# Optimization experiments

Hardware: AMD Instinct MI355X
Metric: run time of the kernel (lower is better)

Reference implementation:

```python
import jax, jax.numpy as jnp
import numpy as np

DIM = 32          # d_model == channel dim of the volume
D_STATE = 16
D_CONV = 4
EXPAND = 2
D_INNER = EXPAND * DIM        # 64
DT_RANK = max(1, (DIM + 15) // 16)  # ceil(d_model/16) = 2
LN_EPS = 1e-5


def setup_inputs() -> dict:
    key = jax.random.key(0)
    ks = jax.random.split(key, 12)
    B, Dd, Hh, Ww = 1, 32, 32, 32
    sc = 0.02
    x = jax.random.normal(ks[0], (B, DIM, Dd, Hh, Ww), jnp.float32)
    ln_w = jnp.ones((DIM,), jnp.float32)
    ln_b = jnp.zeros((DIM,), jnp.float32)
    in_proj_w = jax.random.normal(ks[1], (2 * D_INNER, DIM), jnp.float32) * sc
    conv_w = jax.random.normal(ks[2], (D_INNER, 1, D_CONV), jnp.float32) * sc
    conv_b = jnp.zeros((D_INNER,), jnp.float32)
    x_proj_w = jax.random.normal(ks[3], (DT_RANK + 2 * D_STATE, D_INNER), jnp.float32) * sc
    dt_proj_w = jax.random.normal(ks[4], (D_INNER, DT_RANK), jnp.float32) * sc
    dt_proj_b = jax.random.uniform(ks[5], (D_INNER,), jnp.float32, -4.0, -2.0)  # small softplus(dt) at init
    # Mamba S4D-real init: A = -[1..d_state], stored as A_log
    A_log = jnp.log(jnp.broadcast_to(jnp.arange(1, D_STATE + 1, dtype=jnp.float32), (D_INNER, D_STATE)))
    D_param = jnp.ones((D_INNER,), jnp.float32)
    out_proj_w = jax.random.normal(ks[6], (DIM, D_INNER), jnp.float32) * sc
    return {
        "x": x, "ln_w": ln_w, "ln_b": ln_b, "in_proj_w": in_proj_w,
        "conv_w": conv_w, "conv_b": conv_b, "x_proj_w": x_proj_w,
        "dt_proj_w": dt_proj_w, "dt_proj_b": dt_proj_b, "A_log": A_log,
        "D_param": D_param, "out_proj_w": out_proj_w,
    }


def _mamba_layer(x, ln_w, ln_b, in_proj_w, conv_w, conv_b, x_proj_w,
                 dt_proj_w, dt_proj_b, A_log, D_param, out_proj_w):
    B, C, Dd, Hh, Ww = x.shape
    L = Dd * Hh * Ww
    # z-scan flatten: (B, C, D, H, W) -> (B, L, C)
    xf = x.reshape(B, C, L).transpose(0, 2, 1)
    # LayerNorm over channel dim
    mu = jnp.mean(xf, axis=-1, keepdims=True)
    var = jnp.mean(jnp.square(xf - mu), axis=-1, keepdims=True)
    xn = (xf - mu) * jax.lax.rsqrt(var + LN_EPS) * ln_w + ln_b
    # in_proj -> x, z branches
    xz = xn @ in_proj_w.T                      # (B, L, 2*d_inner)
    x_in, z = jnp.split(xz, 2, axis=-1)
    # depthwise causal conv1d over sequence
    xt = x_in.transpose(0, 2, 1)               # (B, d_inner, L)
    xc = jax.lax.conv_general_dilated(
        xt, conv_w, window_strides=(1,), padding=[(D_CONV - 1, 0)],
        feature_group_count=D_INNER)
    xc = jax.nn.silu(xc + conv_b[None, :, None]).transpose(0, 2, 1)  # (B, L, d_inner)
    # input-dependent dt, B, C
    x_dbl = xc @ x_proj_w.T                    # (B, L, dt_rank + 2*d_state)
    dt, Bm, Cm = jnp.split(x_dbl, [DT_RANK, DT_RANK + D_STATE], axis=-1)
    delta = jax.nn.softplus(dt @ dt_proj_w.T + dt_proj_b)            # (B, L, d_inner)
    A = -jnp.exp(A_log)                        # (d_inner, d_state)
    # discretize: h_t = exp(delta*A) h_{t-1} + delta*B_t*x_t
    dA = jnp.exp(delta[..., None] * A)                               # (B, L, d_inner, d_state)
    dBx = delta[..., None] * Bm[:, :, None, :] * xc[..., None]       # (B, L, d_inner, d_state)
    def comb(e1, e2):
        a1, b1 = e1
        a2, b2 = e2
        return (a1 * a2, a2 * b1 + b2)
    _, h = jax.lax.associative_scan(comb, (dA, dBx), axis=1)         # parallel linear recurrence
    y = jnp.einsum('blds,bls->bld', h, Cm) + xc * D_param            # (B, L, d_inner)
    y = y * jax.nn.silu(z)
    out = y @ out_proj_w.T                     # (B, L, C)
    # unpermute z-scan
    return out.transpose(0, 2, 1).reshape(B, C, Dd, Hh, Ww)


def reference(x, ln_w, ln_b, in_proj_w, conv_w, conv_b, x_proj_w,
              dt_proj_w, dt_proj_b, A_log, D_param, out_proj_w):
    return _mamba_layer(x, ln_w, ln_b, in_proj_w, conv_w, conv_b, x_proj_w,
                        dt_proj_w, dt_proj_b, A_log, D_param, out_proj_w)
```

## Files before the change

### kernel.cpp

```cpp
#include <hip/hip_runtime.h>
#include <hip/hip_bf16.h>

constexpr int L   = 32768;
constexpr int CD  = 32;
constexpr int DI  = 64;
constexpr int DS  = 16;
constexpr int LC  = 64;
constexpr int NCH = L / LC;
constexpr int NPAIR = DI * DS;

constexpr size_t FL        = (size_t)DI * L;
constexpr size_t OFF_SZ    = 0;
constexpr size_t OFF_XC    = FL;
constexpr size_t OFF_DELTA = 2 * FL;
constexpr size_t OFF_BM    = 3 * FL;
constexpr size_t OFF_CM    = OFF_BM + (size_t)DS * L;
constexpr size_t OFF_APROD = OFF_CM + (size_t)DS * L;
constexpr size_t OFF_CARRY = OFF_APROD;
constexpr size_t OFF_BACC  = OFF_APROD + (size_t)NCH * NPAIR;

__device__ __forceinline__ float bf2f(__hip_bfloat16 v) { return __bfloat162float(v); }
__device__ __forceinline__ void f4arr(const float4 v, float* a) { a[0]=v.x; a[1]=v.y; a[2]=v.z; a[3]=v.w; }

__device__ __forceinline__ bool detect_bf16(const void* ln_w) {
    return ((const unsigned short*)ln_w)[0] == 0x3F80;
}
__device__ __forceinline__ float ldin(const void* p, size_t i, bool bf16) {
    return bf16 ? bf2f(((const __hip_bfloat16*)p)[i]) : ((const float*)p)[i];
}

__global__ __launch_bounds__(256) void k12_featurize_scan(
    const void* __restrict__ x,
    const void* __restrict__ ln_w,
    const void* __restrict__ ln_b,
    const void* __restrict__ in_proj_w,
    const void* __restrict__ conv_w,
    const void* __restrict__ conv_b,
    const void* __restrict__ x_proj_w,
    const void* __restrict__ dt_proj_w,
    const void* __restrict__ dt_proj_b,
    const void* __restrict__ A_log,
    float* __restrict__ ws)
{
    __shared__ __align__(16) char smem[67840];
    float (*xin_s)[69]  = (float(*)[69])(smem);
    char* AR = smem + 17664;
    float (*xn_s)[33]   = (float(*)[33])(AR);
    float (*w_in_s)[32] = (float(*)[32])(AR + 8848);
    float (*sdl)[68]    = (float(*)[68])(AR);
    float (*sxc)[68]    = (float(*)[68])(AR + 17408);
    float (*sbm)[68]    = (float(*)[68])(AR + 34816);
    char* FW = smem + 56832;
    float (*w_xp)[64]   = (float(*)[64])(FW);
    float (*w_cv)[4]    = (float(*)[4])(FW + 8704);
    float (*w_dt)[2]    = (float(*)[2])(FW + 9728);
    float* b_dt_s = (float*)(FW + 10240);
    float* b_cv_s = (float*)(FW + 10496);
    float* lnw_s  = (float*)(FW + 10752);
    float* lnb_s  = (float*)(FW + 10880);

    const int tid = threadIdx.x;
    const int l0  = blockIdx.x * LC;
    const bool isb = detect_bf16(ln_w);

    if (isb) {
        const __hip_bfloat16* ipw = (const __hip_bfloat16*)in_proj_w;
        const __hip_bfloat16* xpw = (const __hip_bfloat16*)x_proj_w;
        for (int i = tid; i < 128 * 32; i += 256) w_in_s[i >> 5][i & 31] = bf2f(ipw[i]);
        for (int i = tid; i < 34 * 64; i += 256)  w_xp[i >> 6][i & 63] = bf2f(xpw[i]);
    } else {
        const float* ipw = (const float*)in_proj_w;
        const float* xpw = (const float*)x_proj_w;
        for (int i = tid; i < 128 * 32; i += 256) w_in_s[i >> 5][i & 31] = ipw[i];
        for (int i = tid; i < 34 * 64; i += 256)  w_xp[i >> 6][i & 63] = xpw[i];
    }
    w_cv[tid >> 2][tid & 3] = ldin(conv_w, tid, isb);
    if (tid < 128) w_dt[tid >> 1][tid & 1] = ldin(dt_proj_w, tid, isb);
    if (tid < 64) { b_dt_s[tid] = ldin(dt_proj_b, tid, isb); b_cv_s[tid] = ldin(conv_b, tid, isb); }
    if (tid < 32) { lnw_s[tid] = ldin(ln_w, tid, isb); lnb_s[tid] = ldin(ln_b, tid, isb); }
    __syncthreads();

    if (tid < LC + 3) {
        const int l = l0 - 3 + tid;
        const bool valid = (l >= 0);
        const int lc = valid ? l : 0;
        float xv[CD];
        if (isb) {
            const __hip_bfloat16* xb = (const __hip_bfloat16*)x;
            #pragma unroll
            for (int c = 0; c < CD; ++c) xv[c] = bf2f(xb[(size_t)c * L + lc]);
        } else {
            const float* xf = (const float*)x;
            #pragma unroll
            for (int c = 0; c < CD; ++c) xv[c] = xf[(size_t)c * L + lc];
        }
        float mu = 0.f;
        #pragma unroll
        for (int c = 0; c < CD; ++c) mu += xv[c];
        mu *= (1.f / CD);
        float var = 0.f;
        #pragma unroll
        for (int c = 0; c < CD; ++c) { const float dc = xv[c] - mu; var += dc * dc; }
        const float rstd = rsqrtf(var * (1.f / CD) + 1e-5f);
        #pragma unroll
        for (int c = 0; c < CD; ++c)
            xn_s[tid][c] = valid ? ((xv[c] - mu) * rstd * lnw_s[c] + lnb_s[c]) : 0.f;
    }
    __syncthreads();

    {
        const int wv   = tid >> 6;
        const int lane = tid & 63;
        const int jb   = wv * 32;
        float xv[CD];
        if (wv < 2) {
            #pragma unroll
            for (int it = 0; it < 2; ++it) {
                const int pos = it * 64 + lane;
                if (pos < LC + 3) {
                    #pragma unroll
                    for (int c = 0; c < CD; ++c) xv[c] = xn_s[pos][c];
                    for (int j = 0; j < 32; ++j) {
                        const float4* wr = (const float4*)w_in_s[jb + j];
                        float acc = 0.f;
                        #pragma unroll
                        for (int q = 0; q < 8; ++q) {
                            const float4 w4 = wr[q];
                            acc += w4.x * xv[4*q] + w4.y * xv[4*q+1]
                                 + w4.z * xv[4*q+2] + w4.w * xv[4*q+3];
                        }
                        xin_s[jb + j][pos] = acc;
                    }
                }
            }
        } else {
            const int l = l0 + lane;
            #pragma unroll
            for (int c = 0; c < CD; ++c) xv[c] = xn_s[3 + lane][c];
            for (int j = 0; j < 32; ++j) {
                const float4* wr = (const float4*)w_in_s[jb + j];
                float acc = 0.f;
                #pragma unroll
                for (int q = 0; q < 8; ++q) {
                    const float4 w4 = wr[q];
                    acc += w4.x * xv[4*q] + w4.y * xv[4*q+1]
                         + w4.z * xv[4*q+2] + w4.w * xv[4*q+3];
                }
                const float s = acc / (1.f + __expf(-acc));
                ws[OFF_SZ + (size_t)(jb - 64 + j) * L + l] = s;
            }
        }
    }
    __syncthreads();

    {
        const int h  = tid & 3;
        const int pq = tid >> 2;
        const int l  = l0 + pq;
        const int dbase = h * 16;
        float xcv[16];
        #pragma unroll
        for (int i = 0; i < 16; ++i) {
            const int d = dbase + i;
            float acc = b_cv_s[d];
            #pragma unroll
            for (int k = 0; k < 4; ++k) acc += w_cv[d][k] * xin_s[d][pq + k];
            const float v = acc / (1.f + __expf(-acc));
            xcv[i] = v;
            ws[OFF_XC + (size_t)d * L + l] = v;
            sxc[d][pq] = v;
        }
        float dt0 = 0.f, dt1 = 0.f;
        for (int r = 0; r < 34; ++r) {
            float acc = 0.f;
            #pragma unroll
            for (int i = 0; i < 16; ++i) acc += w_xp[r][dbase + i] * xcv[i];
            acc += __shfl_xor(acc, 1);
            acc += __shfl_xor(acc, 2);
            if (r == 0) dt0 = acc;
            else if (r == 1) dt1 = acc;
            else {
                const int rr = r - 2;
                if (h == (rr >> 3)) {
                    const size_t off = (rr < 16) ? (OFF_BM + (size_t)rr * L)
                                                 : (OFF_CM + (size_t)(rr - 16) * L);
                    ws[off + l] = acc;
                    if (rr < 16) sbm[rr][pq] = acc;
                }
            }
        }
        #pragma unroll
        for (int i = 0; i < 16; ++i) {
            const int d = dbase + i;
            const float tv = dt0 * w_dt[d][0] + dt1 * w_dt[d][1] + b_dt_s[d];
            const float sp = fmaxf(tv, 0.f) + log1pf(__expf(-fabsf(tv)));
            ws[OFF_DELTA + (size_t)d * L + l] = sp;
            sdl[d][pq] = sp;
        }
    }
    __syncthreads();

    {
        const int d = tid >> 2, sg = tid & 3;
        float Aj[4], ap[4] = {1.f, 1.f, 1.f, 1.f}, bb[4] = {0.f, 0.f, 0.f, 0.f};
        #pragma unroll
        for (int j = 0; j < 4; ++j) Aj[j] = -__expf(ldin(A_log, d * DS + sg + 4 * j, isb));

        for (int t = 0; t < LC; t += 4) {
            float ddv[4], xxv[4], bm[4][4];
            f4arr(*(const float4*)&sdl[d][t], ddv);
            f4arr(*(const float4*)&sxc[d][t], xxv);
            f4arr(*(const float4*)&sbm[sg][t],      bm[0]);
            f4arr(*(const float4*)&sbm[sg + 4][t],  bm[1]);
            f4arr(*(const float4*)&sbm[sg + 8][t],  bm[2]);
            f4arr(*(const float4*)&sbm[sg + 12][t], bm[3]);
            #pragma unroll
            for (int tt = 0; tt < 4; ++tt) {
                const float dxc = ddv[tt] * xxv[tt];
                #pragma unroll
                for (int j = 0; j < 4; ++j) {
                    const float e = __expf(ddv[tt] * Aj[j]);
                    ap[j] *= e;
                    bb[j] = e * bb[j] + dxc * bm[j][tt];
                }
            }
        }
        const size_t o = (size_t)blockIdx.x * NPAIR + tid * 4;
        *(float4*)&ws[OFF_APROD + o] = make_float4(ap[0], ap[1], ap[2], ap[3]);
        *(float4*)&ws[OFF_BACC + o]  = make_float4(bb[0], bb[1], bb[2], bb[3]);
    }
}

__global__ __launch_bounds__(256) void k3_carry(float* __restrict__ ws)
{
    const int lane = threadIdx.x & 63;
    const int p    = (blockIdx.x * 256 + threadIdx.x) >> 6;

    float a[8], b[8];
    #pragma unroll
    for (int i = 0; i < 8; ++i) {
        const size_t c = (size_t)(lane * 8 + i);
        a[i] = ws[OFF_APROD + c * NPAIR + p];
        b[i] = ws[OFF_BACC  + c * NPAIR + p];
    }
    float Ag = a[0], Bg = b[0];
    #pragma unroll
    for (int i = 1; i < 8; ++i) { Bg = a[i] * Bg + b[i]; Ag = Ag * a[i]; }
    #pragma unroll
    for (int off = 1; off < 64; off <<= 1) {
        const float pa = __shfl_up(Ag, off);
        const float pb = __shfl_up(Bg, off);
        if (lane >= off) { Bg = Ag * pb + Bg; Ag = Ag * pa; }
    }
    float Pb = __shfl_up(Bg, 1);
    if (lane == 0) Pb = 0.f;
    #pragma unroll
    for (int i = 0; i < 8; ++i) {
        const size_t c = (size_t)(lane * 8 + i);
        ws[OFF_CARRY + c * NPAIR + p] = Pb;
        Pb = a[i] * Pb + b[i];
    }
}

__global__ __launch_bounds__(256) void k45_apply_out(
    const void* __restrict__ A_log,
    const void* __restrict__ D_param,
    const void* __restrict__ ln_w,
    const void* __restrict__ out_proj_w,
    float* __restrict__ ws,
    void* __restrict__ out)
{
    __shared__ __align__(16) float sdl[DI][68];
    __shared__ __align__(16) float sxc[DI][68];
    __shared__ __align__(16) float sbm[DS][68];
    __shared__ __align__(16) float scm[DS][68];
    __shared__ __align__(16) float sy[DI][68];
    __shared__ float w_out_s[CD][DI];
    const int tid = threadIdx.x;
    const int c   = blockIdx.x;
    const size_t t0 = (size_t)c * LC;
    const bool isb = detect_bf16(ln_w);

    if (isb) {
        const __hip_bfloat16* opw = (const __hip_bfloat16*)out_proj_w;
        for (int i = tid; i < CD * DI; i += 256) w_out_s[i >> 6][i & 63] = bf2f(opw[i]);
    } else {
        const float* opw = (const float*)out_proj_w;
        for (int i = tid; i < CD * DI; i += 256) w_out_s[i >> 6][i & 63] = opw[i];
    }
    for (int i = tid; i < DI * LC; i += 256) { const int r = i >> 6, t = i & 63; sdl[r][t] = ws[OFF_DELTA + (size_t)r * L + t0 + t]; }
    for (int i = tid; i < DI * LC; i += 256) { const int r = i >> 6, t = i & 63; sxc[r][t] = ws[OFF_XC + (size_t)r * L + t0 + t]; }
    for (int i = tid; i < DS * LC; i += 256) { const int r = i >> 6, t = i & 63; sbm[r][t] = ws[OFF_BM + (size_t)r * L + t0 + t]; }
    for (int i = tid; i < DS * LC; i += 256) { const int r = i >> 6, t = i & 63; scm[r][t] = ws[OFF_CM + (size_t)r * L + t0 + t]; }

    const int d = tid >> 2, sg = tid & 3;
    float Aj[4];
    #pragma unroll
    for (int j = 0; j < 4; ++j) Aj[j] = -__expf(ldin(A_log, d * DS + sg + 4 * j, isb));
    const float Dd = ldin(D_param, d, isb);
    const float4 h4 = *(const float4*)&ws[OFF_CARRY + (size_t)c * NPAIR + tid * 4];
    float hh[4]; f4arr(h4, hh);
    __syncthreads();

    for (int t = 0; t < LC; t += 4) {
        float ddv[4], xxv[4], bm[4][4], cm[4][4];
        f4arr(*(const float4*)&sdl[d][t], ddv);
        f4arr(*(const float4*)&sxc[d][t], xxv);
        f4arr(*(const float4*)&sbm[sg][t],      bm[0]);
        f4arr(*(const float4*)&sbm[sg + 4][t],  bm[1]);
        f4arr(*(const float4*)&sbm[sg + 8][t],  bm[2]);
        f4arr(*(const float4*)&sbm[sg + 12][t], bm[3]);
        f4arr(*(const float4*)&scm[sg][t],      cm[0]);
        f4arr(*(const float4*)&scm[sg + 4][t],  cm[1]);
        f4arr(*(const float4*)&scm[sg + 8][t],  cm[2]);
        f4arr(*(const float4*)&scm[sg + 12][t], cm[3]);
        #pragma unroll
        for (int tt = 0; tt < 4; ++tt) {
            const float dxc = ddv[tt] * xxv[tt];
            float ys = 0.f;
            #pragma unroll
            for (int j = 0; j < 4; ++j) {
                const float e = __expf(ddv[tt] * Aj[j]);
                hh[j] = e * hh[j] + dxc * bm[j][tt];
                ys += hh[j] * cm[j][tt];
            }
            ys += __shfl_xor(ys, 1);
            ys += __shfl_xor(ys, 2);
            if (sg == 0) sy[d][t + tt] = ys + xxv[tt] * Dd;
        }
    }
    __syncthreads();

    #pragma unroll
    for (int k = 0; k < 4; ++k) {
        const int idx = tid + k * 256;
        const int r = idx >> 4, t4 = (idx & 15) * 4;
        float4 yv = *(float4*)&sy[r][t4];
        const float4 zv = *(const float4*)&ws[OFF_SZ + (size_t)r * L + t0 + t4];
        yv.x *= zv.x; yv.y *= zv.y; yv.z *= zv.z; yv.w *= zv.w;
        *(float4*)&sy[r][t4] = yv;
    }
    __syncthreads();

    {
        const int wv   = tid >> 6;
        const int lane = tid & 63;
        float acc[8] = {0.f, 0.f, 0.f, 0.f, 0.f, 0.f, 0.f, 0.f};
        for (int dd = 0; dd < DI; ++dd) {
            const float yv = sy[dd][lane];
            #pragma unroll
            for (int j = 0; j < 8; ++j)
                acc[j] += yv * w_out_s[wv * 8 + j][dd];
        }
        const size_t l = t0 + lane;
        #pragma unroll
        for (int j = 0; j < 8; ++j) {
            const int cc = wv * 8 + j;
            if (isb) ((__hip_bfloat16*)out)[(size_t)cc * L + l] = __float2bfloat16(acc[j]);
            else     ((float*)out)[(size_t)cc * L + l] = acc[j];
        }
    }
}

extern "C" void kernel_launch(void* const* d_in, const int* in_sizes, int n_in,
                              void* d_out, int out_size, void* d_ws, size_t ws_size,
                              hipStream_t stream)
{
    (void)in_sizes; (void)n_in; (void)out_size; (void)ws_size;
    const void* x        = d_in[0];
    const void* ln_w     = d_in[1];
    const void* ln_b     = d_in[2];
    const void* in_pw    = d_in[3];
    const void* conv_w   = d_in[4];
    const void* conv_b   = d_in[5];
    const void* x_pw     = d_in[6];
    const void* dt_pw    = d_in[7];
    const void* dt_pb    = d_in[8];
    const void* A_log    = d_in[9];
    const void* D_param  = d_in[10];
    const void* out_pw   = d_in[11];
    float* ws = (float*)d_ws;

    k12_featurize_scan<<<NCH, 256, 0, stream>>>(x, ln_w, ln_b, in_pw, conv_w, conv_b,
                                                x_pw, dt_pw, dt_pb, A_log, ws);
    k3_carry<<<NPAIR / 4, 256, 0, stream>>>(ws);
    k45_apply_out<<<NCH, 256, 0, stream>>>(A_log, D_param, ln_w, out_pw, ws, d_out);
}
```

Baseline: 165.7 us.

## Transpose chunk-summary layout, vectorize carry scan, stream delta/xc from global

Chunk summaries (A products and B accumulators) and carries are now stored pair-major (p*NCH + chunk), so the carry kernel reads and writes contiguous float4 rows instead of strided scalars. The apply kernel drops its shared-memory staging of delta and xc and instead prefetches them from global one float4 ahead; it also gains a launch_bounds occupancy hint. In the in_proj stage, each thread now computes two positions per weight-row pass so the weights are read once. The trade-off is strided scalar stores in the chunk kernel and scattered carry loads in the apply kernel, plus global-load latency inside the scan loop.

```diff
diff --git a/kernel.cpp b/kernel.cpp
--- a/kernel.cpp
+++ b/kernel.cpp
@@ -112,29 +112,28 @@
         const int wv   = tid >> 6;
         const int lane = tid & 63;
         const int jb   = wv * 32;
-        float xv[CD];
         if (wv < 2) {
-            #pragma unroll
-            for (int it = 0; it < 2; ++it) {
-                const int pos = it * 64 + lane;
-                if (pos < LC + 3) {
-                    #pragma unroll
-                    for (int c = 0; c < CD; ++c) xv[c] = xn_s[pos][c];
-                    for (int j = 0; j < 32; ++j) {
-                        const float4* wr = (const float4*)w_in_s[jb + j];
-                        float acc = 0.f;
-                        #pragma unroll
-                        for (int q = 0; q < 8; ++q) {
-                            const float4 w4 = wr[q];
-                            acc += w4.x * xv[4*q] + w4.y * xv[4*q+1]
-                                 + w4.z * xv[4*q+2] + w4.w * xv[4*q+3];
-                        }
-                        xin_s[jb + j][pos] = acc;
-                    }
+            const int pos1  = 64 + lane;
+            const bool v1   = (pos1 < LC + 3);
+            const int pos1c = v1 ? pos1 : 66;
+            float xv0[CD], xv1[CD];
+            #pragma unroll
+            for (int c = 0; c < CD; ++c) { xv0[c] = xn_s[lane][c]; xv1[c] = xn_s[pos1c][c]; }
+            for (int j = 0; j < 32; ++j) {
+                const float4* wr = (const float4*)w_in_s[jb + j];
+                float a0 = 0.f, a1 = 0.f;
+                #pragma unroll
+                for (int q = 0; q < 8; ++q) {
+                    const float4 w4 = wr[q];
+                    a0 += w4.x * xv0[4*q] + w4.y * xv0[4*q+1] + w4.z * xv0[4*q+2] + w4.w * xv0[4*q+3];
+                    a1 += w4.x * xv1[4*q] + w4.y * xv1[4*q+1] + w4.z * xv1[4*q+2] + w4.w * xv1[4*q+3];
                 }
+                xin_s[jb + j][lane] = a0;
+                if (v1) xin_s[jb + j][pos1] = a1;
             }
         } else {
             const int l = l0 + lane;
+            float xv[CD];
             #pragma unroll
             for (int c = 0; c < CD; ++c) xv[c] = xn_s[3 + lane][c];
             for (int j = 0; j < 32; ++j) {
@@ -143,8 +142,7 @@
                 #pragma unroll
                 for (int q = 0; q < 8; ++q) {
                     const float4 w4 = wr[q];
-                    acc += w4.x * xv[4*q] + w4.y * xv[4*q+1]
-                         + w4.z * xv[4*q+2] + w4.w * xv[4*q+3];
+                    acc += w4.x * xv[4*q] + w4.y * xv[4*q+1] + w4.z * xv[4*q+2] + w4.w * xv[4*q+3];
                 }
                 const float s = acc / (1.f + __expf(-acc));
                 ws[OFF_SZ + (size_t)(jb - 64 + j) * L + l] = s;
@@ -225,24 +223,28 @@
                 }
             }
         }
-        const size_t o = (size_t)blockIdx.x * NPAIR + tid * 4;
-        *(float4*)&ws[OFF_APROD + o] = make_float4(ap[0], ap[1], ap[2], ap[3]);
-        *(float4*)&ws[OFF_BACC + o]  = make_float4(bb[0], bb[1], bb[2], bb[3]);
+        #pragma unroll
+        for (int j = 0; j < 4; ++j) {
+            const size_t p = (size_t)(tid * 4 + j);
+            ws[OFF_APROD + p * NCH + blockIdx.x] = ap[j];
+            ws[OFF_BACC  + p * NCH + blockIdx.x] = bb[j];
+        }
     }
 }
 
 __global__ __launch_bounds__(256) void k3_carry(float* __restrict__ ws)
 {
     const int lane = threadIdx.x & 63;
-    const int p    = (blockIdx.x * 256 + threadIdx.x) >> 6;
+    const int p    = blockIdx.x * 4 + (threadIdx.x >> 6);
+    const size_t row_a = OFF_APROD + (size_t)p * NCH;
+    const size_t row_b = OFF_BACC  + (size_t)p * NCH;
 
     float a[8], b[8];
-    #pragma unroll
-    for (int i = 0; i < 8; ++i) {
-        const size_t c = (size_t)(lane * 8 + i);
-        a[i] = ws[OFF_APROD + c * NPAIR + p];
-        b[i] = ws[OFF_BACC  + c * NPAIR + p];
-    }
+    f4arr(*(const float4*)&ws[row_a + lane * 8],     a);
+    f4arr(*(const float4*)&ws[row_a + lane * 8 + 4], a + 4);
+    f4arr(*(const float4*)&ws[row_b + lane * 8],     b);
+    f4arr(*(const float4*)&ws[row_b + lane * 8 + 4], b + 4);
+
     float Ag = a[0], Bg = b[0];
     #pragma unroll
     for (int i = 1; i < 8; ++i) { Bg = a[i] * Bg + b[i]; Ag = Ag * a[i]; }
@@ -254,15 +256,14 @@
     }
     float Pb = __shfl_up(Bg, 1);
     if (lane == 0) Pb = 0.f;
-    #pragma unroll
-    for (int i = 0; i < 8; ++i) {
-        const size_t c = (size_t)(lane * 8 + i);
-        ws[OFF_CARRY + c * NPAIR + p] = Pb;
-        Pb = a[i] * Pb + b[i];
-    }
-}
-
-__global__ __launch_bounds__(256) void k45_apply_out(
+    float cr[8];
+    #pragma unroll
+    for (int i = 0; i < 8; ++i) { cr[i] = Pb; Pb = a[i] * Pb + b[i]; }
+    *(float4*)&ws[OFF_CARRY + (size_t)p * NCH + lane * 8]     = make_float4(cr[0], cr[1], cr[2], cr[3]);
+    *(float4*)&ws[OFF_CARRY + (size_t)p * NCH + lane * 8 + 4] = make_float4(cr[4], cr[5], cr[6], cr[7]);
+}
+
+__global__ __launch_bounds__(256, 3) void k45_apply_out(
     const void* __restrict__ A_log,
     const void* __restrict__ D_param,
     const void* __restrict__ ln_w,
@@ -270,8 +271,6 @@
     float* __restrict__ ws,
     void* __restrict__ out)
 {
-    __shared__ __align__(16) float sdl[DI][68];
-    __shared__ __align__(16) float sxc[DI][68];
     __shared__ __align__(16) float sbm[DS][68];
     __shared__ __align__(16) float scm[DS][68];
     __shared__ __align__(16) float sy[DI][68];
@@ -288,24 +287,33 @@
         const float* opw = (const float*)out_proj_w;
         for (int i = tid; i < CD * DI; i += 256) w_out_s[i >> 6][i & 63] = opw[i];
     }
-    for (int i = tid; i < DI * LC; i += 256) { const int r = i >> 6, t = i & 63; sdl[r][t] = ws[OFF_DELTA + (size_t)r * L + t0 + t]; }
-    for (int i = tid; i < DI * LC; i += 256) { const int r = i >> 6, t = i & 63; sxc[r][t] = ws[OFF_XC + (size_t)r * L + t0 + t]; }
-    for (int i = tid; i < DS * LC; i += 256) { const int r = i >> 6, t = i & 63; sbm[r][t] = ws[OFF_BM + (size_t)r * L + t0 + t]; }
-    for (int i = tid; i < DS * LC; i += 256) { const int r = i >> 6, t = i & 63; scm[r][t] = ws[OFF_CM + (size_t)r * L + t0 + t]; }
+    {
+        const int r = tid >> 4, t4 = (tid & 15) * 4;
+        *(float4*)&sbm[r][t4] = *(const float4*)&ws[OFF_BM + (size_t)r * L + t0 + t4];
+        *(float4*)&scm[r][t4] = *(const float4*)&ws[OFF_CM + (size_t)r * L + t0 + t4];
+    }
 
     const int d = tid >> 2, sg = tid & 3;
     float Aj[4];
     #pragma unroll
     for (int j = 0; j < 4; ++j) Aj[j] = -__expf(ldin(A_log, d * DS + sg + 4 * j, isb));
     const float Dd = ldin(D_param, d, isb);
-    const float4 h4 = *(const float4*)&ws[OFF_CARRY + (size_t)c * NPAIR + tid * 4];
-    float hh[4]; f4arr(h4, hh);
-    __syncthreads();
-
+    float hh[4];
+    #pragma unroll
+    for (int j = 0; j < 4; ++j) hh[j] = ws[OFF_CARRY + (size_t)(tid * 4 + j) * NCH + c];
+    __syncthreads();
+
+    const float* dlp = ws + OFF_DELTA + (size_t)d * L + t0;
+    const float* xcp = ws + OFF_XC    + (size_t)d * L + t0;
+    float4 dd4 = *(const float4*)dlp;
+    float4 xx4 = *(const float4*)xcp;
     for (int t = 0; t < LC; t += 4) {
+        const int tn = (t + 4) & 63;
+        const float4 ddn = *(const float4*)(dlp + tn);
+        const float4 xxn = *(const float4*)(xcp + tn);
         float ddv[4], xxv[4], bm[4][4], cm[4][4];
-        f4arr(*(const float4*)&sdl[d][t], ddv);
-        f4arr(*(const float4*)&sxc[d][t], xxv);
+        f4arr(dd4, ddv);
+        f4arr(xx4, xxv);
         f4arr(*(const float4*)&sbm[sg][t],      bm[0]);
         f4arr(*(const float4*)&sbm[sg + 4][t],  bm[1]);
         f4arr(*(const float4*)&sbm[sg + 8][t],  bm[2]);
@@ -328,6 +336,7 @@
             ys += __shfl_xor(ys, 2);
             if (sg == 0) sy[d][t + tt] = ys + xxv[tt] * Dd;
         }
+        dd4 = ddn; xx4 = xxn;
     }
     __syncthreads();
 
```

Measured after the change: 160.6 us. 1.03x faster.
